# Performance work log

Hardware: AMD Instinct MI355X
Metric: run time of the kernel (lower is better)

The kernel has to match this reference:

```python
import jax, jax.numpy as jnp
import numpy as np

V, E, H, A, B, S = 32000, 1024, 1024, 1024, 64, 512

def setup_inputs() -> dict:
    key = jax.random.key(0)
    ks = jax.random.split(key, 20)
    sc = lambda d: 1.0 / np.sqrt(d)
    return {
        "x": jax.random.randint(ks[0], (B,), 0, V),
        "encoder_outputs": jax.random.normal(ks[1], (S, B, H), jnp.float32),
        "h0": jax.random.normal(ks[2], (1, B, H), jnp.float32),
        "c0": jax.random.normal(ks[3], (1, B, H), jnp.float32),
        "Wa": jax.random.normal(ks[4], (A, H), jnp.float32) * sc(H),
        "b_wa": jnp.zeros((A,), jnp.float32),
        "Ua": jax.random.normal(ks[5], (A, H), jnp.float32) * sc(H),
        "b_ua": jnp.zeros((A,), jnp.float32),
        "va": jax.random.normal(ks[6], (1, A), jnp.float32) * sc(A),
        "b_va": jnp.zeros((1,), jnp.float32),
        "emb": jax.random.normal(ks[7], (V, E), jnp.float32) * 0.02,
        "W_ih": jax.random.normal(ks[8], (4 * H, E + H), jnp.float32) * sc(E + H),
        "W_hh": jax.random.normal(ks[9], (4 * H, H), jnp.float32) * sc(H),
        "b_ih": jnp.zeros((4 * H,), jnp.float32),
        "b_hh": jnp.zeros((4 * H,), jnp.float32),
        "W_clf": jax.random.normal(ks[10], (V, H), jnp.float32) * sc(H),
        "b_clf": jnp.zeros((V,), jnp.float32),
    }

def reference(x, encoder_outputs, h0, c0, Wa, b_wa, Ua, b_ua, va, b_va, emb,
              W_ih, W_hh, b_ih, b_hh, W_clf, b_clf):
    # Bahdanau additive attention: scores over time (axis 0)
    tmp1 = jnp.einsum('lbh,ah->lba', h0, Wa) + b_wa            # [1,B,A]
    tmp2 = jnp.einsum('sbh,ah->sba', encoder_outputs, Ua) + b_ua  # [S,B,A]
    scores = jnp.einsum('sba,oa->sbo', jnp.tanh(tmp1 + tmp2), va) + b_va  # [S,B,1]
    w = jax.nn.softmax(scores, axis=0)                          # softmax over S
    ctx = jnp.einsum('sb,sbh->bh', w[..., 0], encoder_outputs)  # [B,H]
    # embed token, concat with context
    inp = jnp.concatenate([emb[x], ctx], axis=-1)               # [B,E+H]
    # single LSTM step (PyTorch gate order i,f,g,o)
    gates = inp @ W_ih.T + b_ih + h0[0] @ W_hh.T + b_hh         # [B,4H]
    i, f, g, o = jnp.split(gates, 4, axis=-1)
    c1 = jax.nn.sigmoid(f) * c0[0] + jax.nn.sigmoid(i) * jnp.tanh(g)
    h1 = jax.nn.sigmoid(o) * jnp.tanh(c1)
    logits = h1 @ W_clf.T + b_clf                               # [B,V]
    return jax.nn.log_softmax(logits, axis=-1)[None]            # [1,B,V]
```

## Files before the change

### kernel.cpp

```cpp
#include <hip/hip_runtime.h>
#include <hip/hip_bf16.h>
#include <math.h>

typedef unsigned short u16;
typedef unsigned int u32;
typedef __attribute__((ext_vector_type(4))) float f32x4;
typedef __attribute__((ext_vector_type(8))) short s16x8;
typedef __attribute__((ext_vector_type(8))) unsigned short u16x8;

#define DEV __device__ __forceinline__


DEV u16 f2bf(float f) {
    union { float f; u32 u; } x{f};
    return (u16)((x.u + 0x7FFFu + ((x.u >> 16) & 1u)) >> 16);
}
DEV float bf2f(u16 h) {
    union { u32 u; float f; } x;
    x.u = ((u32)h) << 16;
    return x.f;
}
DEV float sigm(float x) { return 1.0f / (1.0f + __expf(-x)); }
DEV float tanh_f(float x) {
    float c = fminf(fmaxf(x, -9.0f), 9.0f);
    float e = __expf(2.0f * c);
    return (e - 1.0f) / (e + 1.0f);
}

#define GLL16(g, l) __builtin_amdgcn_global_load_lds( \
    (const __attribute__((address_space(1))) u32*)(g), \
    (__attribute__((address_space(3))) u32*)(l), 16, 0, 0)

__global__ void kzero(float* p, int n) {
    int i = blockIdx.x * blockDim.x + threadIdx.x;
    if (i < n) p[i] = 0.0f;
}

__global__ void kcvt8(const float* __restrict__ in, u16* __restrict__ out, int n8) {
    int i = blockIdx.x * blockDim.x + threadIdx.x;
    if (i >= n8) return;
    float4 f0 = ((const float4*)in)[i * 2];
    float4 f1 = ((const float4*)in)[i * 2 + 1];
    u16x8 o = {f2bf(f0.x), f2bf(f0.y), f2bf(f0.z), f2bf(f0.w),
               f2bf(f1.x), f2bf(f1.y), f2bf(f1.z), f2bf(f1.w)};
    ((u16x8*)out)[i] = o;
}


template<int F0>
DEV void mmq(f32x4 (&acc)[8][4], const s16x8 (&af)[2][2], const s16x8 (&bfrag)[4][2]) {
#pragma unroll
    for (int f = 0; f < 2; f++)
#pragma unroll
        for (int j = 0; j < 4; j++) {
            acc[F0 + f][j] = __builtin_amdgcn_mfma_f32_16x16x32_bf16(af[f][0], bfrag[j][0], acc[F0 + f][j], 0, 0, 0);
            acc[F0 + f][j] = __builtin_amdgcn_mfma_f32_16x16x32_bf16(af[f][1], bfrag[j][1], acc[F0 + f][j], 0, 0, 0);
        }
}

__global__ __launch_bounds__(512, 1) void kscores256v2(
    const u16* __restrict__ encbf, const u16* __restrict__ Uabf,
    const float* __restrict__ tmp1c, const float* __restrict__ va,
    float* __restrict__ scores)
{
    __shared__ __align__(16) u16 shm[65536];

    int wg  = blockIdx.x;
    int lin = (wg & 7) * 64 + (wg >> 3);
    int mt  = lin >> 2, nt = lin & 3;

    int t = threadIdx.x;
    int wid = t >> 6, lane = t & 63;
    int wm = wid >> 2, wn = wid & 3;
    int lr = lane & 15, lg = lane >> 4;

    f32x4 acc[8][4];
#pragma unroll
    for (int i = 0; i < 8; i++)
#pragma unroll
        for (int j = 0; j < 4; j++) acc[i][j] = (f32x4){0.f, 0.f, 0.f, 0.f};

    int srow = t >> 3;
    int sq8  = ((t & 7) ^ (srow & 7)) * 8;
    const u16* asrcb = encbf + (size_t)(mt * 256 + srow) * 1024 + sq8;
    const u16* bsrcb = Uabf + (size_t)(nt * 256 + srow) * 1024 + sq8;

#define STG_A(SE, RB, KO) GLL16(asrcb + (size_t)(RB) * 1024 + (KO), shm + (SE) + (RB) * 64 + t * 8)
#define STG_B(SE, RB, KO) GLL16(bsrcb + (size_t)(RB) * 1024 + (KO), shm + (SE) + 16384 + (RB) * 64 + t * 8)

    const u16* Abase = shm + (wm * 128 + lr) * 64;
    const u16* Bbase = shm + 16384 + (wn * 64 + lr) * 64;
    int xor8 = (lr & 7) * 8;
    int o0 = (lg * 8) ^ xor8;
    int o1 = (32 + lg * 8) ^ xor8;

    s16x8 af[2][2], bfrag[4][2];

#define RD_A2(F0, AB) { \
    af[0][0] = *(const s16x8*)((AB) + (F0) * 1024 + o0); \
    af[0][1] = *(const s16x8*)((AB) + (F0) * 1024 + o1); \
    af[1][0] = *(const s16x8*)((AB) + (F0 + 1) * 1024 + o0); \
    af[1][1] = *(const s16x8*)((AB) + (F0 + 1) * 1024 + o1); }

#define PHTAIL(F0) \
    __builtin_amdgcn_s_barrier(); \
    asm volatile("s_waitcnt lgkmcnt(0)" ::: "memory"); \
    __builtin_amdgcn_sched_barrier(0); \
    __builtin_amdgcn_s_setprio(1); \
    mmq<F0>(acc, af, bfrag); \
    __builtin_amdgcn_s_setprio(0); \
    __builtin_amdgcn_s_barrier(); \
    __builtin_amdgcn_sched_barrier(0);

    STG_B(0, 0, 0);  STG_B(0, 64, 0);  STG_B(0, 128, 0); STG_B(0, 192, 0);
    STG_A(0, 0, 0);  STG_A(0, 128, 0); STG_A(0, 64, 0);  STG_A(0, 192, 0);
    STG_B(32768, 0, 64);  STG_B(32768, 64, 64);
    STG_B(32768, 128, 64); STG_B(32768, 192, 64);
    STG_A(32768, 0, 64);  STG_A(32768, 128, 64);
    asm volatile("s_waitcnt vmcnt(6)" ::: "memory");
    __builtin_amdgcn_s_barrier();
    __builtin_amdgcn_sched_barrier(0);

#define TILE_BODY(T, SB, SBX) { \
    int kA = ((T) + 2 < 16 ? (T) + 2 : 15) * 64; \
    int kH = ((T) + 1 < 16 ? (T) + 1 : 15) * 64; \
    const u16* Ab = Abase + (SB); \
    const u16* Bb = Bbase + (SB); \
     \
    _Pragma("unroll") \
    for (int j = 0; j < 4; j++) { \
        bfrag[j][0] = *(const s16x8*)(Bb + j * 1024 + o0); \
        bfrag[j][1] = *(const s16x8*)(Bb + j * 1024 + o1); \
    } \
    RD_A2(0, Ab); \
    STG_A((SBX), 64, kH); STG_A((SBX), 192, kH); \
    PHTAIL(0); \
     \
    RD_A2(2, Ab); \
    STG_B((SB), 0, kA); STG_B((SB), 64, kA); \
    PHTAIL(2); \
     \
    RD_A2(4, Ab); \
    STG_B((SB), 128, kA); STG_B((SB), 192, kA); \
    PHTAIL(4); \
     \
    RD_A2(6, Ab); \
    STG_A((SB), 0, kA); STG_A((SB), 128, kA); \
    asm volatile("s_waitcnt vmcnt(6)" ::: "memory"); \
    PHTAIL(6); \
}

    for (int tt = 0; tt < 8; tt++) {
        int T0 = tt * 2;
        TILE_BODY(T0, 0, 32768);
        TILE_BODY(T0 + 1, 32768, 0);
    }

    asm volatile("s_waitcnt vmcnt(0)" ::: "memory");
    __builtin_amdgcn_s_barrier();
    __builtin_amdgcn_sched_barrier(0);

    float* ltmp = (float*)shm;
#pragma unroll
    for (int i = 0; i < 8; i++) {
        int idx = t + i * 512;
        int row = idx >> 6, c4 = idx & 63;
        float4 v = *(const float4*)(tmp1c + row * 1024 + nt * 256 + c4 * 4);
        *(float4*)(ltmp + row * 260 + c4 * 4) = v;
    }
    __syncthreads();

    float vaj[4];
#pragma unroll
    for (int j = 0; j < 4; j++) vaj[j] = va[nt * 256 + wn * 64 + j * 16 + lr];

#pragma unroll
    for (int fi = 0; fi < 8; fi++) {
        float rs[4] = {0.f, 0.f, 0.f, 0.f};
#pragma unroll
        for (int j = 0; j < 4; j++) {
            int ac = wn * 64 + j * 16 + lr;
#pragma unroll
            for (int r = 0; r < 4; r++) {
                int b = (fi * 16 + lg * 4 + r) & 63;
                rs[r] += vaj[j] * tanh_f(acc[fi][j][r] + ltmp[b * 260 + ac]);
            }
        }
#pragma unroll
        for (int m = 1; m < 16; m <<= 1)
#pragma unroll
            for (int r = 0; r < 4; r++) rs[r] += __shfl_xor(rs[r], m, 64);
        if (lr == 0) {
            int mrow = mt * 256 + wm * 128 + fi * 16 + lg * 4;
#pragma unroll
            for (int r = 0; r < 4; r++) atomicAdd(&scores[mrow + r], rs[r]);
        }
    }
#undef STG_A
#undef STG_B
#undef RD_A2
#undef PHTAIL
#undef TILE_BODY
}

__global__ __launch_bounds__(256) void kskinny(
    const u16* __restrict__ Abf, int Ktot,
    const float* __restrict__ B1, int K1,
    const float* __restrict__ B2,
    float* __restrict__ Cout, int N, int klen)
{
    __shared__ u16 As[64 * 40];
    __shared__ u16 Bs[128 * 40];

    int nt = blockIdx.x, p = blockIdx.y;
    int t = threadIdx.x;
    int wid = t >> 6, lane = t & 63;
    int lr = lane & 15, lg = lane >> 4;
    int K2 = Ktot - K1;

    f32x4 acc[4][2];
#pragma unroll
    for (int i = 0; i < 4; i++)
#pragma unroll
        for (int j = 0; j < 2; j++) acc[i][j] = (f32x4){0.f, 0.f, 0.f, 0.f};

    int arow = t >> 2, aq = t & 3;
    const u16* ap = Abf + (size_t)arow * Ktot + aq * 8;
    u16* asw = &As[arow * 40 + aq * 8];

    int brow = t >> 1, bhalf = t & 1;
    int n = nt * 128 + brow;
    u16* bsw = &Bs[brow * 40 + bhalf * 16];

    int kbeg = p * klen, kend = kbeg + klen;
    for (int k0 = kbeg; k0 < kend; k0 += 32) {
        __syncthreads();
        *(uint4*)asw = *(const uint4*)(ap + k0);
        int kk = k0 + bhalf * 16;
        const float* bp = (kk < K1) ? (B1 + (size_t)n * K1 + kk)
                                    : (B2 + (size_t)n * K2 + (kk - K1));
        float4 b0 = ((const float4*)bp)[0];
        float4 b1 = ((const float4*)bp)[1];
        float4 b2 = ((const float4*)bp)[2];
        float4 b3 = ((const float4*)bp)[3];
        u16x8 q0 = {f2bf(b0.x), f2bf(b0.y), f2bf(b0.z), f2bf(b0.w),
                    f2bf(b1.x), f2bf(b1.y), f2bf(b1.z), f2bf(b1.w)};
        u16x8 q1 = {f2bf(b2.x), f2bf(b2.y), f2bf(b2.z), f2bf(b2.w),
                    f2bf(b3.x), f2bf(b3.y), f2bf(b3.z), f2bf(b3.w)};
        *(u16x8*)bsw = q0;
        *(u16x8*)(bsw + 8) = q1;
        __syncthreads();

        const u16* abase = &As[lr * 40 + lg * 8];
        const u16* bbase = &Bs[(wid * 32 + lr) * 40 + lg * 8];
        s16x8 af[4], bfr[2];
#pragma unroll
        for (int i = 0; i < 4; i++) af[i]  = *(const s16x8*)(abase + i * 16 * 40);
#pragma unroll
        for (int j = 0; j < 2; j++) bfr[j] = *(const s16x8*)(bbase + j * 16 * 40);
#pragma unroll
        for (int i = 0; i < 4; i++)
#pragma unroll
            for (int j = 0; j < 2; j++)
                acc[i][j] = __builtin_amdgcn_mfma_f32_16x16x32_bf16(af[i], bfr[j], acc[i][j], 0, 0, 0);
    }

#pragma unroll
    for (int i = 0; i < 4; i++)
#pragma unroll
        for (int j = 0; j < 2; j++) {
            int m = i * 16 + lg * 4;
            int col = nt * 128 + wid * 32 + j * 16 + lr;
#pragma unroll
            for (int r = 0; r < 4; r++)
                Cout[((size_t)(p * 64 + m + r)) * N + col] = acc[i][j][r];
        }
}

__global__ void kredbias(const float* __restrict__ part, const float* __restrict__ bias1,
                         const float* __restrict__ bias2, float* __restrict__ out,
                         int N, int P)
{
    int idx = blockIdx.x * blockDim.x + threadIdx.x;
    if (idx >= 64 * N) return;
    int n = idx % N;
    float v = bias1[n] + bias2[n];
    for (int p = 0; p < P; p++) v += part[(size_t)p * 64 * N + idx];
    out[idx] = v;
}

__global__ __launch_bounds__(512) void ksoftmax_w(const float* __restrict__ scores,
                                                  float* __restrict__ w)
{
    int b = blockIdx.x, s = threadIdx.x;
    __shared__ float red[8], red2[8];
    float v = scores[s * 64 + b];
    float m = v;
#pragma unroll
    for (int mask = 1; mask < 64; mask <<= 1) m = fmaxf(m, __shfl_xor(m, mask, 64));
    if ((s & 63) == 0) red[s >> 6] = m;
    __syncthreads();
#pragma unroll
    for (int k = 0; k < 8; k++) m = fmaxf(m, red[k]);
    float e = __expf(v - m);
    float sum = e;
#pragma unroll
    for (int mask = 1; mask < 64; mask <<= 1) sum += __shfl_xor(sum, mask, 64);
    if ((s & 63) == 0) red2[s >> 6] = sum;
    __syncthreads();
    sum = 0.f;
#pragma unroll
    for (int k = 0; k < 8; k++) sum += red2[k];
    w[s * 64 + b] = e / sum;
}

__global__ __launch_bounds__(256) void kctx(const u16* __restrict__ encbf,
                                            const float* __restrict__ w,
                                            float* __restrict__ pctx)
{
    int b = blockIdx.x & 63, ch = blockIdx.x >> 6;
    int h4 = threadIdx.x;
    float4 acc = {0.f, 0.f, 0.f, 0.f};
    int s0 = ch * 64;
#pragma unroll 4
    for (int si = 0; si < 64; si++) {
        int s = s0 + si;
        float wv = w[s * 64 + b];
        ushort4 e = ((const ushort4*)(encbf + ((size_t)(s * 64 + b)) * 1024))[h4];
        acc.x += wv * bf2f(e.x); acc.y += wv * bf2f(e.y);
        acc.z += wv * bf2f(e.z); acc.w += wv * bf2f(e.w);
    }
    ((float4*)pctx)[((size_t)(ch * 64 + b)) * 256 + h4] = acc;
}

__global__ void kbuild(const int* __restrict__ x, const float* __restrict__ emb,
                       const float* __restrict__ pctx, const float* __restrict__ h0,
                       u16* __restrict__ inp2bf)
{
    int idx = blockIdx.x * blockDim.x + threadIdx.x;
    if (idx >= 64 * 3072) return;
    int b = idx / 3072, k = idx % 3072;
    float v;
    if (k < 1024) {
        v = emb[(size_t)x[b] * 1024 + k];
    } else if (k < 2048) {
        int h = k - 1024;
        v = 0.f;
        for (int p = 0; p < 8; p++) v += pctx[(size_t)(p * 64 + b) * 1024 + h];
    } else {
        v = h0[b * 1024 + (k - 2048)];
    }
    inp2bf[idx] = f2bf(v);
}

__global__ void klstm(const float* __restrict__ gp, const float* __restrict__ b_ih,
                      const float* __restrict__ b_hh, const float* __restrict__ c0,
                      u16* __restrict__ h1bf)
{
    int idx = blockIdx.x * blockDim.x + threadIdx.x;
    int b = idx >> 10, j = idx & 1023;
    float ig = b_ih[j] + b_hh[j];
    float fg = b_ih[1024 + j] + b_hh[1024 + j];
    float gg = b_ih[2048 + j] + b_hh[2048 + j];
    float og = b_ih[3072 + j] + b_hh[3072 + j];
    for (int p = 0; p < 8; p++) {
        const float* g = gp + ((size_t)p * 64 + b) * 4096;
        ig += g[j]; fg += g[1024 + j]; gg += g[2048 + j]; og += g[3072 + j];
    }
    float c = sigm(fg) * c0[idx] + sigm(ig) * tanh_f(gg);
    float h = sigm(og) * tanh_f(c);
    h1bf[idx] = f2bf(h);
}

__global__ __launch_bounds__(1024) void klogsoftmax(const float* __restrict__ lp,
                                                    const float* __restrict__ b_clf,
                                                    float* __restrict__ out)
{
    int b = blockIdx.x, t = threadIdx.x;
    __shared__ float red[16], red2[16];
    float v[32];
    float mx = -1e30f;
#pragma unroll
    for (int i = 0; i < 32; i++) {
        int idx = t + i * 1024;
        if (idx < 32000) {
            float s = b_clf[idx];
#pragma unroll
            for (int p = 0; p < 4; p++)
                s += lp[((size_t)(p * 64 + b)) * 32000 + idx];
            v[i] = s;
            mx = fmaxf(mx, v[i]);
        } else v[i] = -1e30f;
    }
#pragma unroll
    for (int mask = 1; mask < 64; mask <<= 1) mx = fmaxf(mx, __shfl_xor(mx, mask, 64));
    if ((t & 63) == 0) red[t >> 6] = mx;
    __syncthreads();
#pragma unroll
    for (int k = 0; k < 16; k++) mx = fmaxf(mx, red[k]);
    float s = 0.f;
#pragma unroll
    for (int i = 0; i < 32; i++) {
        int idx = t + i * 1024;
        if (idx < 32000) s += __expf(v[i] - mx);
    }
#pragma unroll
    for (int mask = 1; mask < 64; mask <<= 1) s += __shfl_xor(s, mask, 64);
    if ((t & 63) == 0) red2[t >> 6] = s;
    __syncthreads();
    s = 0.f;
#pragma unroll
    for (int k = 0; k < 16; k++) s += red2[k];
    float lse = mx + logf(s);
#pragma unroll
    for (int i = 0; i < 32; i++) {
        int idx = t + i * 1024;
        if (idx < 32000) out[(size_t)b * 32000 + idx] = v[i] - lse;
    }
}

extern "C" void kernel_launch(void* const* d_in, const int* in_sizes, int n_in,
                              void* d_out, int out_size, void* d_ws, size_t ws_size,
                              hipStream_t stream)
{
    const int*   x     = (const int*)d_in[0];
    const float* enc   = (const float*)d_in[1];
    const float* h0    = (const float*)d_in[2];
    const float* c0    = (const float*)d_in[3];
    const float* Wa    = (const float*)d_in[4];
    const float* b_wa  = (const float*)d_in[5];
    const float* Ua    = (const float*)d_in[6];
    const float* b_ua  = (const float*)d_in[7];
    const float* va    = (const float*)d_in[8];
    const float* emb   = (const float*)d_in[10];
    const float* W_ih  = (const float*)d_in[11];
    const float* W_hh  = (const float*)d_in[12];
    const float* b_ih  = (const float*)d_in[13];
    const float* b_hh  = (const float*)d_in[14];
    const float* W_clf = (const float*)d_in[15];
    const float* b_clf = (const float*)d_in[16];
    float* out = (float*)d_out;

    char* ws = (char*)d_ws;
    u16*   encbf    = (u16*)  (ws + 0);
    float* gparts   = (float*)(ws + 0);
    float* lparts   = (float*)(ws + 8388608);
    float* scores   = (float*)(ws + 67108864);
    float* wbuf     = (float*)(ws + 67239936);
    float* tmp1part = (float*)(ws + 67371008);
    float* tmp1c    = (float*)(ws + 69468160);
    u16*   h0bf     = (u16*)  (ws + 69730304);
    u16*   Uabf     = (u16*)  (ws + 69861376);
    float* pctx     = (float*)(ws + 71958528);
    u16*   inp2bf   = (u16*)  (ws + 74055680);
    u16*   h1bf     = (u16*)  (ws + 74448896);

    kzero<<<128, 256, 0, stream>>>(scores, 32768);
    kcvt8<<<16384, 256, 0, stream>>>(enc, encbf, 33554432 / 8);
    kcvt8<<<512, 256, 0, stream>>>(Ua, Uabf, 1048576 / 8);
    kcvt8<<<32, 256, 0, stream>>>(h0, h0bf, 65536 / 8);

    {
        dim3 g(8, 8);
        kskinny<<<g, 256, 0, stream>>>(h0bf, 1024, Wa, 1024, nullptr, tmp1part, 1024, 128);
    }
    kredbias<<<256, 256, 0, stream>>>(tmp1part, b_wa, b_ua, tmp1c, 1024, 8);

    kscores256v2<<<512, 512, 0, stream>>>(encbf, Uabf, tmp1c, va, scores);
    ksoftmax_w<<<64, 512, 0, stream>>>(scores, wbuf);
    kctx<<<512, 256, 0, stream>>>(encbf, wbuf, pctx);
    kbuild<<<768, 256, 0, stream>>>(x, emb, pctx, h0, inp2bf);

    {
        dim3 g(32, 8);
        kskinny<<<g, 256, 0, stream>>>(inp2bf, 3072, W_ih, 2048, W_hh, gparts, 4096, 384);
    }
    klstm<<<256, 256, 0, stream>>>(gparts, b_ih, b_hh, c0, h1bf);

    {
        dim3 g(250, 4);
        kskinny<<<g, 256, 0, stream>>>(h1bf, 1024, W_clf, 1024, nullptr, lparts, 32000, 256);
    }
    klogsoftmax<<<64, 1024, 0, stream>>>(lparts, b_clf, out);
}
```

Baseline: 233.2 us.

## Fuse prep kernels, reschedule scores GEMM barriers, halve classifier K-split

Three small prep launches (zeroing scores, converting Ua and h0 to bf16) are merged into one kernel to cut launch overhead. The scores GEMM main loop issues its global-to-LDS stage loads before the fragment reads, drops the explicit lgkmcnt wait, and removes one of the two barriers per phase. Some phases now keep no barrier at all, which relaxes synchronisation but could race on LDS reuse. The classifier GEMM splits K two ways instead of four, so log-softmax sums fewer partials, at the cost of fewer blocks and longer per-block loops.

```diff
diff --git a/kernel.cpp b/kernel.cpp
--- a/kernel.cpp
+++ b/kernel.cpp
@@ -30,11 +30,6 @@
 #define GLL16(g, l) __builtin_amdgcn_global_load_lds( \
     (const __attribute__((address_space(1))) u32*)(g), \
     (__attribute__((address_space(3))) u32*)(l), 16, 0, 0)
-
-__global__ void kzero(float* p, int n) {
-    int i = blockIdx.x * blockDim.x + threadIdx.x;
-    if (i < n) p[i] = 0.0f;
-}
 
 __global__ void kcvt8(const float* __restrict__ in, u16* __restrict__ out, int n8) {
     int i = blockIdx.x * blockDim.x + threadIdx.x;
@@ -46,6 +41,32 @@
     ((u16x8*)out)[i] = o;
 }
 
+__global__ __launch_bounds__(256) void kprep(
+    const float* __restrict__ Ua, const float* __restrict__ h0,
+    u16* __restrict__ Uabf, u16* __restrict__ h0bf, float* __restrict__ scores)
+{
+    int bid = blockIdx.x, t = threadIdx.x;
+    if (bid < 16) {
+        int i = bid * 2048 + t * 8;
+        *(float4*)(scores + i) = (float4){0.f, 0.f, 0.f, 0.f};
+        *(float4*)(scores + i + 4) = (float4){0.f, 0.f, 0.f, 0.f};
+    } else if (bid < 528) {
+        int i = (bid - 16) * 256 + t;
+        float4 f0 = ((const float4*)Ua)[i * 2];
+        float4 f1 = ((const float4*)Ua)[i * 2 + 1];
+        u16x8 o = {f2bf(f0.x), f2bf(f0.y), f2bf(f0.z), f2bf(f0.w),
+                   f2bf(f1.x), f2bf(f1.y), f2bf(f1.z), f2bf(f1.w)};
+        ((u16x8*)Uabf)[i] = o;
+    } else {
+        int i = (bid - 528) * 256 + t;
+        float4 f0 = ((const float4*)h0)[i * 2];
+        float4 f1 = ((const float4*)h0)[i * 2 + 1];
+        u16x8 o = {f2bf(f0.x), f2bf(f0.y), f2bf(f0.z), f2bf(f0.w),
+                   f2bf(f1.x), f2bf(f1.y), f2bf(f1.z), f2bf(f1.w)};
+        ((u16x8*)h0bf)[i] = o;
+    }
+}
+
 
 template<int F0>
 DEV void mmq(f32x4 (&acc)[8][4], const s16x8 (&af)[2][2], const s16x8 (&bfrag)[4][2]) {
@@ -102,13 +123,12 @@
     af[1][0] = *(const s16x8*)((AB) + (F0 + 1) * 1024 + o0); \
     af[1][1] = *(const s16x8*)((AB) + (F0 + 1) * 1024 + o1); }
 
-#define PHTAIL(F0) \
-    __builtin_amdgcn_s_barrier(); \
-    asm volatile("s_waitcnt lgkmcnt(0)" ::: "memory"); \
-    __builtin_amdgcn_sched_barrier(0); \
+#define MM(F0) \
     __builtin_amdgcn_s_setprio(1); \
     mmq<F0>(acc, af, bfrag); \
-    __builtin_amdgcn_s_setprio(0); \
+    __builtin_amdgcn_s_setprio(0);
+
+#define BAR() \
     __builtin_amdgcn_s_barrier(); \
     __builtin_amdgcn_sched_barrier(0);
 
@@ -118,8 +138,7 @@
     STG_B(32768, 128, 64); STG_B(32768, 192, 64);
     STG_A(32768, 0, 64);  STG_A(32768, 128, 64);
     asm volatile("s_waitcnt vmcnt(6)" ::: "memory");
-    __builtin_amdgcn_s_barrier();
-    __builtin_amdgcn_sched_barrier(0);
+    BAR();
 
 #define TILE_BODY(T, SB, SBX) { \
     int kA = ((T) + 2 < 16 ? (T) + 2 : 15) * 64; \
@@ -127,27 +146,31 @@
     const u16* Ab = Abase + (SB); \
     const u16* Bb = Bbase + (SB); \
      \
+    STG_A((SBX), 64, kH); STG_A((SBX), 192, kH); \
     _Pragma("unroll") \
     for (int j = 0; j < 4; j++) { \
         bfrag[j][0] = *(const s16x8*)(Bb + j * 1024 + o0); \
         bfrag[j][1] = *(const s16x8*)(Bb + j * 1024 + o1); \
     } \
     RD_A2(0, Ab); \
-    STG_A((SBX), 64, kH); STG_A((SBX), 192, kH); \
-    PHTAIL(0); \
+    MM(0); \
+    BAR();                       \
      \
+    STG_B((SB), 0, kA); STG_B((SB), 64, kA); \
     RD_A2(2, Ab); \
-    STG_B((SB), 0, kA); STG_B((SB), 64, kA); \
-    PHTAIL(2); \
+    MM(2); \
+    __builtin_amdgcn_sched_barrier(0); \
      \
+    STG_B((SB), 128, kA); STG_B((SB), 192, kA); \
     RD_A2(4, Ab); \
-    STG_B((SB), 128, kA); STG_B((SB), 192, kA); \
-    PHTAIL(4); \
+    MM(4); \
+    BAR();                       \
      \
+    STG_A((SB), 0, kA); STG_A((SB), 128, kA); \
     RD_A2(6, Ab); \
-    STG_A((SB), 0, kA); STG_A((SB), 128, kA); \
     asm volatile("s_waitcnt vmcnt(6)" ::: "memory"); \
-    PHTAIL(6); \
+    MM(6); \
+    BAR();                       \
 }
 
     for (int tt = 0; tt < 8; tt++) {
@@ -199,7 +222,8 @@
 #undef STG_A
 #undef STG_B
 #undef RD_A2
-#undef PHTAIL
+#undef MM
+#undef BAR
 #undef TILE_BODY
 }
 
@@ -386,7 +410,7 @@
         if (idx < 32000) {
             float s = b_clf[idx];
 #pragma unroll
-            for (int p = 0; p < 4; p++)
+            for (int p = 0; p < 2; p++)
                 s += lp[((size_t)(p * 64 + b)) * 32000 + idx];
             v[i] = s;
             mx = fmaxf(mx, v[i]);
@@ -455,10 +479,8 @@
     u16*   inp2bf   = (u16*)  (ws + 74055680);
     u16*   h1bf     = (u16*)  (ws + 74448896);
 
-    kzero<<<128, 256, 0, stream>>>(scores, 32768);
+    kprep<<<560, 256, 0, stream>>>(Ua, h0, Uabf, h0bf, scores);
     kcvt8<<<16384, 256, 0, stream>>>(enc, encbf, 33554432 / 8);
-    kcvt8<<<512, 256, 0, stream>>>(Ua, Uabf, 1048576 / 8);
-    kcvt8<<<32, 256, 0, stream>>>(h0, h0bf, 65536 / 8);
 
     {
         dim3 g(8, 8);
@@ -478,8 +500,8 @@
     klstm<<<256, 256, 0, stream>>>(gparts, b_ih, b_hh, c0, h1bf);
 
     {
-        dim3 g(250, 4);
-        kskinny<<<g, 256, 0, stream>>>(h1bf, 1024, W_clf, 1024, nullptr, lparts, 32000, 256);
+        dim3 g(250, 2);
+        kskinny<<<g, 256, 0, stream>>>(h1bf, 1024, W_clf, 1024, nullptr, lparts, 32000, 512);
     }
     klogsoftmax<<<64, 1024, 0, stream>>>(lparts, b_clf, out);
 }
```

Measured after the change: 219.3 us. -5.9%, faster.
